# Performance work log

Measured on AMD Instinct MI355X. Metric: run time of the kernel, lower is better.

Reference implementation:

```python
import jax, jax.numpy as jnp
import numpy as np

N_NODES = 100000
N_EDGES = 400000
N_GRAPHS = 4096
IN_DIM = 128
HID = 64
HEADS = 8
NEG_SLOPE = 0.2


def setup_inputs() -> dict:
    key = jax.random.key(0)
    ks = jax.random.split(key, 12)
    x = jax.random.normal(ks[0], (N_NODES, IN_DIM), dtype=jnp.float32)
    edge_index = jax.random.randint(ks[1], (2, N_EDGES), 0, N_NODES, dtype=jnp.int64)
    batch = jnp.sort(jax.random.randint(ks[2], (N_NODES,), 0, N_GRAPHS, dtype=jnp.int64))
    s = 1.0 / np.sqrt(IN_DIM)
    W1 = jax.random.normal(ks[3], (IN_DIM, HEADS * HID), dtype=jnp.float32) * s
    att_src1 = jax.random.normal(ks[4], (HEADS, HID), dtype=jnp.float32) * 0.1
    att_dst1 = jax.random.normal(ks[5], (HEADS, HID), dtype=jnp.float32) * 0.1
    b1 = jnp.zeros((HEADS * HID,), dtype=jnp.float32)
    s2 = 1.0 / np.sqrt(HEADS * HID)
    W2 = jax.random.normal(ks[6], (HEADS * HID, HID), dtype=jnp.float32) * s2
    att_src2 = jax.random.normal(ks[7], (1, HID), dtype=jnp.float32) * 0.1
    att_dst2 = jax.random.normal(ks[8], (1, HID), dtype=jnp.float32) * 0.1
    b2 = jnp.zeros((HID,), dtype=jnp.float32)
    Wf = jax.random.normal(ks[9], (HID, 1), dtype=jnp.float32) * (1.0 / np.sqrt(HID))
    bf = jnp.zeros((1,), dtype=jnp.float32)
    return {"x": x, "edge_index": edge_index, "batch": batch,
            "W1": W1, "att_src1": att_src1, "att_dst1": att_dst1, "b1": b1,
            "W2": W2, "att_src2": att_src2, "att_dst2": att_dst2, "b2": b2,
            "Wf": Wf, "bf": bf}


def _gat_layer(x, src, dst, W, att_src, att_dst, bias, heads, out_ch, concat):
    # PyG GATConv math (add_self_loops handled by caller via src/dst)
    n = x.shape[0]
    h = (x @ W).reshape(n, heads, out_ch)          # [N, H, C]
    a_s = (h * att_src[None]).sum(-1)               # [N, H]
    a_d = (h * att_dst[None]).sum(-1)               # [N, H]
    alpha = a_s[src] + a_d[dst]                     # [E, H]
    alpha = jax.nn.leaky_relu(alpha, NEG_SLOPE)
    amax = jax.ops.segment_max(alpha, dst, num_segments=n)
    alpha = jnp.exp(alpha - amax[dst])
    denom = jax.ops.segment_sum(alpha, dst, num_segments=n)
    alpha = alpha / (denom[dst] + 1e-16)
    msg = h[src] * alpha[:, :, None]                # [E, H, C]
    out = jax.ops.segment_sum(msg, dst, num_segments=n)  # [N, H, C]
    out = out.reshape(n, heads * out_ch) if concat else out.mean(axis=1)
    return out + bias


def reference(x, edge_index, batch, W1, att_src1, att_dst1, b1,
              W2, att_src2, att_dst2, b2, Wf, bf):
    n = x.shape[0]
    loop = jnp.arange(n, dtype=edge_index.dtype)
    src = jnp.concatenate([edge_index[0], loop])
    dst = jnp.concatenate([edge_index[1], loop])
    h = _gat_layer(x, src, dst, W1, att_src1, att_dst1, b1, HEADS, HID, True)
    h = jax.nn.relu(h)
    h = _gat_layer(h, src, dst, W2, att_src2, att_dst2, b2, 1, HID, False)
    h = jax.nn.relu(h)
    sums = jax.ops.segment_sum(h, batch, num_segments=N_GRAPHS)        # [G, HID]
    cnts = jax.ops.segment_sum(jnp.ones((n,), h.dtype), batch, num_segments=N_GRAPHS)
    pooled = sums / jnp.clip(cnts, 1.0)[:, None]
    return pooled @ Wf + bf
```

## Files before the change

### kernel.cpp

```cpp
#include <hip/hip_runtime.h>

typedef short bfrag8 __attribute__((ext_vector_type(8)));
typedef float f32x4 __attribute__((ext_vector_type(4)));
typedef unsigned int uint4v __attribute__((ext_vector_type(4)));

#define SCAN_BLK 2048

__device__ __forceinline__ unsigned short f2bf(float f) {
    unsigned u = __float_as_uint(f);
    u += 0x7fffu + ((u >> 16) & 1u);
    return (unsigned short)(u >> 16);
}
__device__ __forceinline__ float bf2f(unsigned short s) {
    return __uint_as_float((unsigned)s << 16);
}
__device__ __forceinline__ bfrag8 pack8(float4 a, float4 b) {
    bfrag8 r;
    r[0] = (short)f2bf(a.x); r[1] = (short)f2bf(a.y);
    r[2] = (short)f2bf(a.z); r[3] = (short)f2bf(a.w);
    r[4] = (short)f2bf(b.x); r[5] = (short)f2bf(b.y);
    r[6] = (short)f2bf(b.z); r[7] = (short)f2bf(b.w);
    return r;
}

__global__ __launch_bounds__(256) void prologue(int* __restrict__ cnt,
                                                const float* __restrict__ W1,
                                                const float* __restrict__ W2,
                                                unsigned short* __restrict__ wf1,
                                                unsigned short* __restrict__ wf2,
                                                const int* __restrict__ batch,
                                                int* __restrict__ gstart,
                                                int* __restrict__ rs,
                                                int N, int G, int E) {
    const int b = blockIdx.x, t = threadIdx.x;
    if (b < 512) {
        int i = b * 256 + t;
        if (i < N) cnt[i] = 0;
    } else if (b < 768) {
        int i = (b - 512) * 256 + t;
        int e = i & 7, l = (i >> 3) & 63, c = (i >> 9) & 3, s = (i >> 11) & 3, h = i >> 13;
        int k = s * 32 + (l >> 4) * 8 + e;
        int col = h * 64 + c * 16 + (l & 15);
        wf1[i] = f2bf(W1[k * 512 + col]);
    } else if (b < 896) {
        int i = (b - 768) * 256 + t;
        int e = i & 7, l = (i >> 3) & 63, c = (i >> 9) & 3, s = i >> 11;
        int k = s * 32 + (l >> 4) * 8 + e;
        int col = c * 16 + (l & 15);
        wf2[i] = f2bf(W2[k * 64 + col]);
    } else {
        int i = (b - 896) * 256 + t;
        if (i == 0) rs[N] = E + N;
        if (i > N) return;
        if (i == N) {
            int p = batch[N - 1];
            for (int g = p + 1; g <= G; ++g) gstart[g] = N;
        } else {
            int bb = batch[i];
            int p = (i == 0) ? -1 : batch[i - 1];
            for (int g = p + 1; g <= bb; ++g) gstart[g] = i;
        }
    }
}

__global__ __launch_bounds__(256) void gemm_l1_hist(const float* __restrict__ x,
                                                    const unsigned short* __restrict__ Bfrag,
                                                    unsigned short* __restrict__ Cbf,
                                                    int M,
                                                    const float* __restrict__ avs,
                                                    const float* __restrict__ avd,
                                                    float* __restrict__ as_,
                                                    float* __restrict__ ad_,
                                                    int gemmBlocks,
                                                    const int* __restrict__ ei,
                                                    int* __restrict__ cnt, int E) {
    const int b = blockIdx.x;
    if (b >= gemmBlocks) {
        int t = (b - gemmBlocks) * 256 + threadIdx.x;
        if (t < E + M) {
            int dst = (t < E) ? ei[E + t] : t - E;
            atomicAdd(cnt + dst, 1);
        }
        return;
    }
    const int lane = threadIdx.x & 63;
    const int wave = threadIdx.x >> 6;
    const int l15 = lane & 15, l16 = lane >> 4;
    const long rowBase = (long)b * 128 + wave * 32;

    long r0 = rowBase + l15;        if (r0 > M - 1) r0 = M - 1;
    long r1 = rowBase + 16 + l15;   if (r1 > M - 1) r1 = M - 1;

    bfrag8 a0f[4], a1f[4];
#pragma unroll
    for (int s = 0; s < 4; ++s) {
        const float* p0 = x + r0 * 128 + s * 32 + l16 * 8;
        const float* p1 = x + r1 * 128 + s * 32 + l16 * 8;
        float4 u0 = *(const float4*)p0, u1 = *(const float4*)(p0 + 4);
        float4 v0 = *(const float4*)p1, v1 = *(const float4*)(p1 + 4);
        a0f[s] = pack8(u0, u1);
        a1f[s] = pack8(v0, v1);
    }

#pragma unroll 1
    for (int h = 0; h < 8; ++h) {
        bfrag8 bf[4][4];
        const bfrag8* bp = (const bfrag8*)(Bfrag + (size_t)h * 8192);
#pragma unroll
        for (int s = 0; s < 4; ++s)
#pragma unroll
            for (int c = 0; c < 4; ++c)
                bf[s][c] = bp[(s * 4 + c) * 64 + lane];

        f32x4 acc[2][4];
#pragma unroll
        for (int r = 0; r < 2; ++r)
#pragma unroll
            for (int c = 0; c < 4; ++c)
#pragma unroll
                for (int e = 0; e < 4; ++e) acc[r][c][e] = 0.f;

#pragma unroll
        for (int s = 0; s < 4; ++s) {
#pragma unroll
            for (int c = 0; c < 4; ++c) {
                acc[0][c] = __builtin_amdgcn_mfma_f32_16x16x32_bf16(a0f[s], bf[s][c], acc[0][c], 0, 0, 0);
                acc[1][c] = __builtin_amdgcn_mfma_f32_16x16x32_bf16(a1f[s], bf[s][c], acc[1][c], 0, 0, 0);
            }
        }

        float avsv[4], avdv[4];
#pragma unroll
        for (int c = 0; c < 4; ++c) {
            avsv[c] = avs[h * 64 + c * 16 + l15];
            avdv[c] = avd[h * 64 + c * 16 + l15];
        }

#pragma unroll
        for (int r = 0; r < 2; ++r) {
#pragma unroll
            for (int reg = 0; reg < 4; ++reg) {
                long row = rowBase + r * 16 + l16 * 4 + reg;
                bool ok = row < M;
                float ps = 0.f, pd = 0.f;
#pragma unroll
                for (int c = 0; c < 4; ++c) {
                    float v = acc[r][c][reg];
                    if (ok) Cbf[row * 512 + h * 64 + c * 16 + l15] = f2bf(v);
                    ps += v * avsv[c];
                    pd += v * avdv[c];
                }
#pragma unroll
                for (int off = 1; off < 16; off <<= 1) {
                    ps += __shfl_xor(ps, off);
                    pd += __shfl_xor(pd, off);
                }
                if (l15 == 0 && ok) {
                    as_[row * 8 + h] = ps;
                    ad_[row * 8 + h] = pd;
                }
            }
        }
    }
}

__global__ __launch_bounds__(256) void scan1(const int* __restrict__ cnt,
                                             int* __restrict__ rs,
                                             int* __restrict__ bsum, int N) {
    __shared__ int lds[256];
    int base = blockIdx.x * SCAN_BLK;
    int vals[8];
    int tsum = 0;
    int idx0 = base + threadIdx.x * 8;
#pragma unroll
    for (int j = 0; j < 8; ++j) {
        int i = idx0 + j;
        int v = (i < N) ? cnt[i] : 0;
        vals[j] = tsum;
        tsum += v;
    }
    lds[threadIdx.x] = tsum;
    __syncthreads();
    for (int off = 1; off < 256; off <<= 1) {
        int v = lds[threadIdx.x];
        int u = (threadIdx.x >= (unsigned)off) ? lds[threadIdx.x - off] : 0;
        __syncthreads();
        lds[threadIdx.x] = v + u;
        __syncthreads();
    }
    int texcl = (threadIdx.x == 0) ? 0 : lds[threadIdx.x - 1];
#pragma unroll
    for (int j = 0; j < 8; ++j) {
        int i = idx0 + j;
        if (i < N) rs[i] = texcl + vals[j];
    }
    if (threadIdx.x == 255) bsum[blockIdx.x] = lds[255];
}

__global__ __launch_bounds__(256) void scan_fix(int* __restrict__ rs,
                                                const int* __restrict__ bsum, int N) {
    __shared__ int sprefix;
    int b = blockIdx.x;
    int i = b * 256 + threadIdx.x;
    int chunk = (b * 256) / SCAN_BLK;
    if (threadIdx.x == 0) {
        int p = 0;
        for (int k = 0; k < chunk; ++k) p += bsum[k];
        sprefix = p;
    }
    __syncthreads();
    if (i < N) rs[i] += sprefix;
}

__global__ __launch_bounds__(256) void scatter_cd(const int* __restrict__ ei,
                                                  const int* __restrict__ rs,
                                                  int* __restrict__ cnt,
                                                  int* __restrict__ csrc, int E, int N) {
    int t = (int)(blockIdx.x * 256u + threadIdx.x);
    if (t >= E + N) return;
    int src, dst;
    if (t < E) { src = ei[t]; dst = ei[E + t]; } else { src = dst = t - E; }
    int pos = rs[dst] + atomicSub(cnt + dst, 1) - 1;
    csrc[pos] = src;
}

__global__ __launch_bounds__(256) void gather8(const int* __restrict__ csrc,
                                               const int* __restrict__ rs,
                                               const float* __restrict__ as_,
                                               const float* __restrict__ ad_,
                                               const unsigned short* __restrict__ h,
                                               const float* __restrict__ bias,
                                               unsigned short* __restrict__ outp,
                                               int N) {
    int node = (int)((blockIdx.x * 256u + threadIdx.x) >> 6);
    int lane = threadIdx.x & 63;
    if (node >= N) return;
    int myh = lane >> 3;
    int s0 = rs[node], s1 = rs[node + 1];
    float adn = ad_[(size_t)node * 8 + myh];
    float den = 0.f;
    float2 acc[4] = {};
    const unsigned* hu = (const unsigned*)h;
    for (int k = s0; k < s1; k += 4) {
        int k1 = k + 1 < s1 ? k + 1 : s0;
        int k2 = k + 2 < s1 ? k + 2 : s0;
        int k3 = k + 3 < s1 ? k + 3 : s0;
        bool m1 = k + 1 < s1, m2 = k + 2 < s1, m3 = k + 3 < s1;
        int i0 = csrc[k], i1 = csrc[k1], i2 = csrc[k2], i3 = csrc[k3];
        float a0 = as_[(size_t)i0 * 8 + myh] + adn;
        float a1 = as_[(size_t)i1 * 8 + myh] + adn;
        float a2 = as_[(size_t)i2 * 8 + myh] + adn;
        float a3 = as_[(size_t)i3 * 8 + myh] + adn;
        a0 = a0 > 0.f ? a0 : 0.2f * a0;  a1 = a1 > 0.f ? a1 : 0.2f * a1;
        a2 = a2 > 0.f ? a2 : 0.2f * a2;  a3 = a3 > 0.f ? a3 : 0.2f * a3;
        float w0 = __expf(fminf(a0, 60.f));
        float w1 = m1 ? __expf(fminf(a1, 60.f)) : 0.f;
        float w2 = m2 ? __expf(fminf(a2, 60.f)) : 0.f;
        float w3 = m3 ? __expf(fminf(a3, 60.f)) : 0.f;
        uint4v v0 = *(const uint4v*)(hu + (size_t)i0 * 256 + lane * 4);
        uint4v v1 = *(const uint4v*)(hu + (size_t)i1 * 256 + lane * 4);
        uint4v v2 = *(const uint4v*)(hu + (size_t)i2 * 256 + lane * 4);
        uint4v v3 = *(const uint4v*)(hu + (size_t)i3 * 256 + lane * 4);
        den += (w0 + w1) + (w2 + w3);
#pragma unroll
        for (int j = 0; j < 4; ++j) {
            acc[j].x += w0 * __uint_as_float(v0[j] << 16);
            acc[j].y += w0 * __uint_as_float(v0[j] & 0xffff0000u);
            acc[j].x += w1 * __uint_as_float(v1[j] << 16);
            acc[j].y += w1 * __uint_as_float(v1[j] & 0xffff0000u);
            acc[j].x += w2 * __uint_as_float(v2[j] << 16);
            acc[j].y += w2 * __uint_as_float(v2[j] & 0xffff0000u);
            acc[j].x += w3 * __uint_as_float(v3[j] << 16);
            acc[j].y += w3 * __uint_as_float(v3[j] & 0xffff0000u);
        }
    }
    float rden = 1.f / (den + 1e-16f);
    uint4v o;
#pragma unroll
    for (int j = 0; j < 4; ++j) {
        float vlo = acc[j].x * rden + bias[lane * 8 + 2 * j];
        float vhi = acc[j].y * rden + bias[lane * 8 + 2 * j + 1];
        vlo = vlo > 0.f ? vlo : 0.f;
        vhi = vhi > 0.f ? vhi : 0.f;
        o[j] = (unsigned)f2bf(vlo) | ((unsigned)f2bf(vhi) << 16);
    }
    *(uint4v*)(outp + (size_t)node * 512 + lane * 8) = o;
}

__global__ __launch_bounds__(256) void gemm_l2_k512(const unsigned short* __restrict__ A,
                                                    const unsigned short* __restrict__ Bfrag,
                                                    unsigned short* __restrict__ Cbf,
                                                    int M,
                                                    const float* __restrict__ avs,
                                                    const float* __restrict__ avd,
                                                    float* __restrict__ as_,
                                                    float* __restrict__ ad_) {
    const int lane = threadIdx.x & 63;
    const int wave = threadIdx.x >> 6;
    const int l15 = lane & 15, l16 = lane >> 4;
    const long rowBase = (long)blockIdx.x * 128 + wave * 32;
    const bfrag8* bp = (const bfrag8*)Bfrag;

    f32x4 acc[2][4];
#pragma unroll
    for (int r = 0; r < 2; ++r)
#pragma unroll
        for (int c = 0; c < 4; ++c)
#pragma unroll
            for (int e = 0; e < 4; ++e) acc[r][c][e] = 0.f;

    long r0 = rowBase + l15;        if (r0 > M - 1) r0 = M - 1;
    long r1 = rowBase + 16 + l15;   if (r1 > M - 1) r1 = M - 1;
    const unsigned short* a0p = A + r0 * 512 + l16 * 8;
    const unsigned short* a1p = A + r1 * 512 + l16 * 8;

    for (int s = 0; s < 16; ++s) {
        bfrag8 a0 = *(const bfrag8*)(a0p + s * 32);
        bfrag8 a1 = *(const bfrag8*)(a1p + s * 32);
        bfrag8 bf0 = bp[(s * 4 + 0) * 64 + lane];
        bfrag8 bf1 = bp[(s * 4 + 1) * 64 + lane];
        bfrag8 bf2 = bp[(s * 4 + 2) * 64 + lane];
        bfrag8 bf3 = bp[(s * 4 + 3) * 64 + lane];
        acc[0][0] = __builtin_amdgcn_mfma_f32_16x16x32_bf16(a0, bf0, acc[0][0], 0, 0, 0);
        acc[1][0] = __builtin_amdgcn_mfma_f32_16x16x32_bf16(a1, bf0, acc[1][0], 0, 0, 0);
        acc[0][1] = __builtin_amdgcn_mfma_f32_16x16x32_bf16(a0, bf1, acc[0][1], 0, 0, 0);
        acc[1][1] = __builtin_amdgcn_mfma_f32_16x16x32_bf16(a1, bf1, acc[1][1], 0, 0, 0);
        acc[0][2] = __builtin_amdgcn_mfma_f32_16x16x32_bf16(a0, bf2, acc[0][2], 0, 0, 0);
        acc[1][2] = __builtin_amdgcn_mfma_f32_16x16x32_bf16(a1, bf2, acc[1][2], 0, 0, 0);
        acc[0][3] = __builtin_amdgcn_mfma_f32_16x16x32_bf16(a0, bf3, acc[0][3], 0, 0, 0);
        acc[1][3] = __builtin_amdgcn_mfma_f32_16x16x32_bf16(a1, bf3, acc[1][3], 0, 0, 0);
    }

    float avsv[4], avdv[4];
#pragma unroll
    for (int c = 0; c < 4; ++c) {
        avsv[c] = avs[c * 16 + l15];
        avdv[c] = avd[c * 16 + l15];
    }

#pragma unroll
    for (int r = 0; r < 2; ++r) {
#pragma unroll
        for (int reg = 0; reg < 4; ++reg) {
            long row = rowBase + r * 16 + l16 * 4 + reg;
            bool ok = row < M;
            float ps = 0.f, pd = 0.f;
#pragma unroll
            for (int c = 0; c < 4; ++c) {
                float v = acc[r][c][reg];
                if (ok) Cbf[row * 64 + c * 16 + l15] = f2bf(v);
                ps += v * avsv[c];
                pd += v * avdv[c];
            }
#pragma unroll
            for (int off = 1; off < 16; off <<= 1) {
                ps += __shfl_xor(ps, off);
                pd += __shfl_xor(pd, off);
            }
            if (l15 == 0 && ok) { as_[row] = ps; ad_[row] = pd; }
        }
    }
}

__global__ __launch_bounds__(256) void gather1(const int* __restrict__ csrc,
                                               const int* __restrict__ rs,
                                               const float* __restrict__ as_,
                                               const float* __restrict__ ad_,
                                               const unsigned short* __restrict__ h,
                                               const float* __restrict__ bias,
                                               float* __restrict__ outp, int N) {
    int node = (int)((blockIdx.x * 256u + threadIdx.x) >> 6);
    int lane = threadIdx.x & 63;
    if (node >= N) return;
    int s0 = rs[node], s1 = rs[node + 1];
    float adn = ad_[node];
    float den = 0.f, acc = 0.f;
    for (int k = s0; k < s1; k += 4) {
        int k1 = k + 1 < s1 ? k + 1 : s0;
        int k2 = k + 2 < s1 ? k + 2 : s0;
        int k3 = k + 3 < s1 ? k + 3 : s0;
        bool m1 = k + 1 < s1, m2 = k + 2 < s1, m3 = k + 3 < s1;
        int i0 = csrc[k], i1 = csrc[k1], i2 = csrc[k2], i3 = csrc[k3];
        float a0 = as_[i0] + adn, a1 = as_[i1] + adn, a2 = as_[i2] + adn, a3 = as_[i3] + adn;
        a0 = a0 > 0.f ? a0 : 0.2f * a0;  a1 = a1 > 0.f ? a1 : 0.2f * a1;
        a2 = a2 > 0.f ? a2 : 0.2f * a2;  a3 = a3 > 0.f ? a3 : 0.2f * a3;
        float w0 = __expf(fminf(a0, 60.f));
        float w1 = m1 ? __expf(fminf(a1, 60.f)) : 0.f;
        float w2 = m2 ? __expf(fminf(a2, 60.f)) : 0.f;
        float w3 = m3 ? __expf(fminf(a3, 60.f)) : 0.f;
        float h0 = bf2f(h[(size_t)i0 * 64 + lane]);
        float h1 = bf2f(h[(size_t)i1 * 64 + lane]);
        float h2 = bf2f(h[(size_t)i2 * 64 + lane]);
        float h3 = bf2f(h[(size_t)i3 * 64 + lane]);
        den += (w0 + w1) + (w2 + w3);
        acc += w0 * h0;  acc += w1 * h1;  acc += w2 * h2;  acc += w3 * h3;
    }
    float v = acc / (den + 1e-16f) + bias[lane];
    outp[(size_t)node * 64 + lane] = v > 0.f ? v : 0.f;
}

__global__ __launch_bounds__(256) void pool_readout(const float* __restrict__ h2,
                                                    const int* __restrict__ gstart,
                                                    const float* __restrict__ Wf,
                                                    const float* __restrict__ bf,
                                                    float* __restrict__ out, int G) {
    int g = (int)((blockIdx.x * 256u + threadIdx.x) >> 6);
    int lane = threadIdx.x & 63;
    if (g >= G) return;
    int s0 = gstart[g], s1 = gstart[g + 1];
    float acc = 0.f;
    int i = s0;
    for (; i + 2 <= s1; i += 2) {
        acc += h2[(size_t)i * 64 + lane];
        acc += h2[(size_t)(i + 1) * 64 + lane];
    }
    if (i < s1) acc += h2[(size_t)i * 64 + lane];
    float c = (float)(s1 - s0);
    c = c < 1.f ? 1.f : c;
    float v = acc / c * Wf[lane];
#pragma unroll
    for (int off = 32; off; off >>= 1) v += __shfl_xor(v, off);
    if (lane == 0) out[g] = v + bf[0];
}

extern "C" void kernel_launch(void* const* d_in, const int* in_sizes, int n_in,
                              void* d_out, int out_size, void* d_ws, size_t ws_size,
                              hipStream_t stream) {
    const float* x        = (const float*)d_in[0];
    const int*   ei       = (const int*)d_in[1];
    const int*   batch    = (const int*)d_in[2];
    const float* W1       = (const float*)d_in[3];
    const float* att_src1 = (const float*)d_in[4];
    const float* att_dst1 = (const float*)d_in[5];
    const float* b1       = (const float*)d_in[6];
    const float* W2       = (const float*)d_in[7];
    const float* att_src2 = (const float*)d_in[8];
    const float* att_dst2 = (const float*)d_in[9];
    const float* b2       = (const float*)d_in[10];
    const float* Wf       = (const float*)d_in[11];
    const float* bf       = (const float*)d_in[12];
    float* out = (float*)d_out;

    const int N = in_sizes[2];
    const int E = in_sizes[1] / 2;
    const int G = out_size;

    const int nb = (N + SCAN_BLK - 1) / SCAN_BLK;
    const int nodeWaveGrid = (int)(((size_t)N * 64 + 255) / 256);
    const int edgeGrid = (E + N + 255) / 256;
    const int gemmGrid = (N + 127) / 128;

    char* base = (char*)d_ws;
    size_t off = 0;
    auto alloc = [&](size_t bytes) { char* p = base + off; off += (bytes + 255) & ~255llu; return p; };
    unsigned short* wf1   = (unsigned short*)alloc(131072);
    unsigned short* wf2   = (unsigned short*)alloc(65536);
    float* as1            = (float*)alloc((size_t)N * 8 * 4);
    float* ad1            = (float*)alloc((size_t)N * 8 * 4);
    float* as2            = (float*)alloc((size_t)N * 4);
    float* ad2            = (float*)alloc((size_t)N * 4);
    int*   cnt_i          = (int*)alloc((size_t)N * 4);
    int*   rs             = (int*)alloc((size_t)(N + 1) * 4);
    int*   csrc           = (int*)alloc((size_t)(E + N) * 4);
    int*   bsum           = (int*)alloc(1024);
    int*   gstart         = (int*)alloc((size_t)(G + 1) * 4);
    float* ob2            = (float*)alloc((size_t)N * 64 * 4);
    unsigned short* h2bf  = (unsigned short*)alloc((size_t)N * 64 * 2);
    unsigned short* h1_bf = (unsigned short*)alloc((size_t)N * 512 * 2);
    unsigned short* ob1_bf= (unsigned short*)alloc((size_t)N * 512 * 2);
    (void)ws_size;

    {
        int gsBlocks = (N + 256) / 256 + 1;
        prologue<<<896 + gsBlocks, 256, 0, stream>>>(cnt_i, W1, W2, wf1, wf2,
                                                     batch, gstart, rs, N, G, E);
    }

    gemm_l1_hist<<<gemmGrid + edgeGrid, 256, 0, stream>>>(
        x, wf1, h1_bf, N, att_src1, att_dst1, as1, ad1,
        gemmGrid, ei, cnt_i, E);

    scan1<<<nb, 256, 0, stream>>>(cnt_i, rs, bsum, N);
    scan_fix<<<(N + 255) / 256, 256, 0, stream>>>(rs, bsum, N);
    scatter_cd<<<edgeGrid, 256, 0, stream>>>(ei, rs, cnt_i, csrc, E, N);

    gather8<<<nodeWaveGrid, 256, 0, stream>>>(csrc, rs, as1, ad1, h1_bf, b1, ob1_bf, N);

    gemm_l2_k512<<<gemmGrid, 256, 0, stream>>>(ob1_bf, wf2, h2bf, N,
                                               att_src2, att_dst2, as2, ad2);

    gather1<<<nodeWaveGrid, 256, 0, stream>>>(csrc, rs, as2, ad2, h2bf, b2, ob2, N);

    pool_readout<<<(G * 64 + 255) / 256, 256, 0, stream>>>(ob2, gstart, Wf, bf, out, G);
}
```

Baseline: 282.4 us.

## Fuse layer-2 gather with mean-pool readout via atomics; add scalar tail loops

The layer-2 gather now projects each node's output onto Wf, divides by the graph's node count, and atomically adds it into the per-graph output. The output is pre-initialised with the bias in the prologue. This removes the fp32 N×64 intermediate buffer and the separate pool kernel, at the cost of one atomic per node and a change in summation order. Both gather kernels also replace the masked, clamped 4-wide remainder handling with a clean 4-wide main loop plus a scalar tail, avoiding redundant loads and exps.

Measured after the change: 297.0 us. 5.2% more time.

```diff
diff --git a/kernel.cpp b/kernel.cpp
--- a/kernel.cpp
+++ b/kernel.cpp
@@ -28,6 +28,8 @@
                                                 const float* __restrict__ W2,
                                                 unsigned short* __restrict__ wf1,
                                                 unsigned short* __restrict__ wf2,
+                                                const float* __restrict__ bf,
+                                                float* __restrict__ out,
                                                 const int* __restrict__ batch,
                                                 int* __restrict__ gstart,
                                                 int* __restrict__ rs,
@@ -48,8 +50,11 @@
         int k = s * 32 + (l >> 4) * 8 + e;
         int col = c * 16 + (l & 15);
         wf2[i] = f2bf(W2[k * 64 + col]);
+    } else if (b < 912) {
+        int i = (b - 896) * 256 + t;
+        if (i < G) out[i] = bf[0];
     } else {
-        int i = (b - 896) * 256 + t;
+        int i = (b - 912) * 256 + t;
         if (i == 0) rs[N] = E + N;
         if (i > N) return;
         if (i == N) {
@@ -241,22 +246,17 @@
     float den = 0.f;
     float2 acc[4] = {};
     const unsigned* hu = (const unsigned*)h;
-    for (int k = s0; k < s1; k += 4) {
-        int k1 = k + 1 < s1 ? k + 1 : s0;
-        int k2 = k + 2 < s1 ? k + 2 : s0;
-        int k3 = k + 3 < s1 ? k + 3 : s0;
-        bool m1 = k + 1 < s1, m2 = k + 2 < s1, m3 = k + 3 < s1;
-        int i0 = csrc[k], i1 = csrc[k1], i2 = csrc[k2], i3 = csrc[k3];
+    int k = s0;
+    for (; k + 4 <= s1; k += 4) {
+        int i0 = csrc[k], i1 = csrc[k + 1], i2 = csrc[k + 2], i3 = csrc[k + 3];
         float a0 = as_[(size_t)i0 * 8 + myh] + adn;
         float a1 = as_[(size_t)i1 * 8 + myh] + adn;
         float a2 = as_[(size_t)i2 * 8 + myh] + adn;
         float a3 = as_[(size_t)i3 * 8 + myh] + adn;
         a0 = a0 > 0.f ? a0 : 0.2f * a0;  a1 = a1 > 0.f ? a1 : 0.2f * a1;
         a2 = a2 > 0.f ? a2 : 0.2f * a2;  a3 = a3 > 0.f ? a3 : 0.2f * a3;
-        float w0 = __expf(fminf(a0, 60.f));
-        float w1 = m1 ? __expf(fminf(a1, 60.f)) : 0.f;
-        float w2 = m2 ? __expf(fminf(a2, 60.f)) : 0.f;
-        float w3 = m3 ? __expf(fminf(a3, 60.f)) : 0.f;
+        float w0 = __expf(fminf(a0, 60.f)), w1 = __expf(fminf(a1, 60.f));
+        float w2 = __expf(fminf(a2, 60.f)), w3 = __expf(fminf(a3, 60.f));
         uint4v v0 = *(const uint4v*)(hu + (size_t)i0 * 256 + lane * 4);
         uint4v v1 = *(const uint4v*)(hu + (size_t)i1 * 256 + lane * 4);
         uint4v v2 = *(const uint4v*)(hu + (size_t)i2 * 256 + lane * 4);
@@ -272,6 +272,19 @@
             acc[j].y += w2 * __uint_as_float(v2[j] & 0xffff0000u);
             acc[j].x += w3 * __uint_as_float(v3[j] << 16);
             acc[j].y += w3 * __uint_as_float(v3[j] & 0xffff0000u);
+        }
+    }
+    for (; k < s1; ++k) {
+        int i0 = csrc[k];
+        float a = as_[(size_t)i0 * 8 + myh] + adn;
+        a = a > 0.f ? a : 0.2f * a;
+        float w = __expf(fminf(a, 60.f));
+        uint4v v0 = *(const uint4v*)(hu + (size_t)i0 * 256 + lane * 4);
+        den += w;
+#pragma unroll
+        for (int j = 0; j < 4; ++j) {
+            acc[j].x += w * __uint_as_float(v0[j] << 16);
+            acc[j].y += w * __uint_as_float(v0[j] & 0xffff0000u);
         }
     }
     float rden = 1.f / (den + 1e-16f);
@@ -362,32 +375,30 @@
     }
 }
 
-__global__ __launch_bounds__(256) void gather1(const int* __restrict__ csrc,
-                                               const int* __restrict__ rs,
-                                               const float* __restrict__ as_,
-                                               const float* __restrict__ ad_,
-                                               const unsigned short* __restrict__ h,
-                                               const float* __restrict__ bias,
-                                               float* __restrict__ outp, int N) {
+__global__ __launch_bounds__(256) void gather1_pool(const int* __restrict__ csrc,
+                                                    const int* __restrict__ rs,
+                                                    const float* __restrict__ as_,
+                                                    const float* __restrict__ ad_,
+                                                    const unsigned short* __restrict__ h,
+                                                    const float* __restrict__ bias,
+                                                    const int* __restrict__ batch,
+                                                    const int* __restrict__ gstart,
+                                                    const float* __restrict__ Wf,
+                                                    float* __restrict__ out, int N) {
     int node = (int)((blockIdx.x * 256u + threadIdx.x) >> 6);
     int lane = threadIdx.x & 63;
     if (node >= N) return;
     int s0 = rs[node], s1 = rs[node + 1];
     float adn = ad_[node];
     float den = 0.f, acc = 0.f;
-    for (int k = s0; k < s1; k += 4) {
-        int k1 = k + 1 < s1 ? k + 1 : s0;
-        int k2 = k + 2 < s1 ? k + 2 : s0;
-        int k3 = k + 3 < s1 ? k + 3 : s0;
-        bool m1 = k + 1 < s1, m2 = k + 2 < s1, m3 = k + 3 < s1;
-        int i0 = csrc[k], i1 = csrc[k1], i2 = csrc[k2], i3 = csrc[k3];
+    int k = s0;
+    for (; k + 4 <= s1; k += 4) {
+        int i0 = csrc[k], i1 = csrc[k + 1], i2 = csrc[k + 2], i3 = csrc[k + 3];
         float a0 = as_[i0] + adn, a1 = as_[i1] + adn, a2 = as_[i2] + adn, a3 = as_[i3] + adn;
         a0 = a0 > 0.f ? a0 : 0.2f * a0;  a1 = a1 > 0.f ? a1 : 0.2f * a1;
         a2 = a2 > 0.f ? a2 : 0.2f * a2;  a3 = a3 > 0.f ? a3 : 0.2f * a3;
-        float w0 = __expf(fminf(a0, 60.f));
-        float w1 = m1 ? __expf(fminf(a1, 60.f)) : 0.f;
-        float w2 = m2 ? __expf(fminf(a2, 60.f)) : 0.f;
-        float w3 = m3 ? __expf(fminf(a3, 60.f)) : 0.f;
+        float w0 = __expf(fminf(a0, 60.f)), w1 = __expf(fminf(a1, 60.f));
+        float w2 = __expf(fminf(a2, 60.f)), w3 = __expf(fminf(a3, 60.f));
         float h0 = bf2f(h[(size_t)i0 * 64 + lane]);
         float h1 = bf2f(h[(size_t)i1 * 64 + lane]);
         float h2 = bf2f(h[(size_t)i2 * 64 + lane]);
@@ -395,32 +406,24 @@
         den += (w0 + w1) + (w2 + w3);
         acc += w0 * h0;  acc += w1 * h1;  acc += w2 * h2;  acc += w3 * h3;
     }
+    for (; k < s1; ++k) {
+        int i0 = csrc[k];
+        float a = as_[i0] + adn;
+        a = a > 0.f ? a : 0.2f * a;
+        float w = __expf(fminf(a, 60.f));
+        den += w;
+        acc += w * bf2f(h[(size_t)i0 * 64 + lane]);
+    }
     float v = acc / (den + 1e-16f) + bias[lane];
-    outp[(size_t)node * 64 + lane] = v > 0.f ? v : 0.f;
-}
-
-__global__ __launch_bounds__(256) void pool_readout(const float* __restrict__ h2,
-                                                    const int* __restrict__ gstart,
-                                                    const float* __restrict__ Wf,
-                                                    const float* __restrict__ bf,
-                                                    float* __restrict__ out, int G) {
-    int g = (int)((blockIdx.x * 256u + threadIdx.x) >> 6);
-    int lane = threadIdx.x & 63;
-    if (g >= G) return;
-    int s0 = gstart[g], s1 = gstart[g + 1];
-    float acc = 0.f;
-    int i = s0;
-    for (; i + 2 <= s1; i += 2) {
-        acc += h2[(size_t)i * 64 + lane];
-        acc += h2[(size_t)(i + 1) * 64 + lane];
-    }
-    if (i < s1) acc += h2[(size_t)i * 64 + lane];
-    float c = (float)(s1 - s0);
-    c = c < 1.f ? 1.f : c;
-    float v = acc / c * Wf[lane];
-#pragma unroll
-    for (int off = 32; off; off >>= 1) v += __shfl_xor(v, off);
-    if (lane == 0) out[g] = v + bf[0];
+    v = v > 0.f ? v : 0.f;
+    float s = v * Wf[lane];
+#pragma unroll
+    for (int off = 32; off; off >>= 1) s += __shfl_xor(s, off);
+    if (lane == 0) {
+        int b = batch[node];
+        float cnt = (float)(gstart[b + 1] - gstart[b]);
+        atomicAdd(out + b, s / cnt);
+    }
 }
 
 extern "C" void kernel_launch(void* const* d_in, const int* in_sizes, int n_in,
@@ -464,7 +467,6 @@
     int*   csrc           = (int*)alloc((size_t)(E + N) * 4);
     int*   bsum           = (int*)alloc(1024);
     int*   gstart         = (int*)alloc((size_t)(G + 1) * 4);
-    float* ob2            = (float*)alloc((size_t)N * 64 * 4);
     unsigned short* h2bf  = (unsigned short*)alloc((size_t)N * 64 * 2);
     unsigned short* h1_bf = (unsigned short*)alloc((size_t)N * 512 * 2);
     unsigned short* ob1_bf= (unsigned short*)alloc((size_t)N * 512 * 2);
@@ -472,8 +474,8 @@
 
     {
         int gsBlocks = (N + 256) / 256 + 1;
-        prologue<<<896 + gsBlocks, 256, 0, stream>>>(cnt_i, W1, W2, wf1, wf2,
-                                                     batch, gstart, rs, N, G, E);
+        prologue<<<912 + gsBlocks, 256, 0, stream>>>(cnt_i, W1, W2, wf1, wf2,
+                                                     bf, out, batch, gstart, rs, N, G, E);
     }
 
     gemm_l1_hist<<<gemmGrid + edgeGrid, 256, 0, stream>>>(
@@ -489,7 +491,6 @@
     gemm_l2_k512<<<gemmGrid, 256, 0, stream>>>(ob1_bf, wf2, h2bf, N,
                                                att_src2, att_dst2, as2, ad2);
 
-    gather1<<<nodeWaveGrid, 256, 0, stream>>>(csrc, rs, as2, ad2, h2bf, b2, ob2, N);
-
-    pool_readout<<<(G * 64 + 255) / 256, 256, 0, stream>>>(ob2, gstart, Wf, bf, out, G);
-}
+    gather1_pool<<<nodeWaveGrid, 256, 0, stream>>>(csrc, rs, as2, ad2, h2bf, b2,
+                                                   batch, gstart, Wf, out, N);
+}
```
